# Kernel tuning notes

Hardware: AMD Instinct MI355X
Metric: run time of the kernel (lower is better)

## Reference

```python
import jax, jax.numpy as jnp
import numpy as np

B, T, I, H, L, S = 128, 256, 256, 256, 4, 3


def _gru(x_t, w_i, b_i, b_h):
    # torch.nn.GRUCell called WITHOUT hx in the source => hidden state is 0,
    # so Whh @ 0 vanishes and only the b_hh bias contributes to the gates.
    gi = x_t @ w_i.T + b_i                      # [B, 3H]
    hh = b_h.shape[0] // 3
    i_r, i_z, i_n = gi[:, :hh], gi[:, hh:2 * hh], gi[:, 2 * hh:]
    h_r, h_z, h_n = b_h[:hh], b_h[hh:2 * hh], b_h[2 * hh:]
    r = jax.nn.sigmoid(i_r + h_r)
    z = jax.nn.sigmoid(i_z + h_z)
    n = jnp.tanh(i_n + r * h_n)
    return (1.0 - z) * n                        # + z * 0


def setup_inputs() -> dict:
    key = jax.random.key(0)
    ks = jax.random.split(key, 12)
    s = 1.0 / np.sqrt(H)
    u = lambda k, shape: jax.random.uniform(k, shape, jnp.float32, -s, s)
    return {
        "x": jax.random.normal(ks[0], (B, T, I), jnp.float32),
        "hidden": jax.random.normal(ks[1], (B, L, L), jnp.float32),
        "w_ih0": u(ks[2], (S, 3 * H, I)),      # layer-0 input weights, per split
        "b_ih0": u(ks[3], (S, 3 * H)),
        "b_hh0": u(ks[4], (S, 3 * H)),
        "w_ih": u(ks[5], (S, L - 1, 3 * H, H)),  # layers 1..L-1
        "b_ih": u(ks[6], (S, L - 1, 3 * H)),
        "b_hh": u(ks[7], (S, L - 1, 3 * H)),
        "w_lw": u(ks[8], (L, H)),              # layer_weights: Linear(H -> L)
        "b_lw": u(ks[9], (L,)),
        "w_sel": u(ks[10], (S, H + I)),        # selective_layer: Linear(H+I -> S)
        "b_sel": u(ks[11], (S,)),
    }


def reference(x, hidden, w_ih0, b_ih0, b_hh0, w_ih, b_ih, b_hh, w_lw, b_lw, w_sel, b_sel):
    Lm1 = w_ih.shape[1]

    def run_stack(x_t, cur):
        # cur is a (possibly traced) int index selecting one of S GRU stacks
        hs = [_gru(x_t, w_ih0[cur], b_ih0[cur], b_hh0[cur])]
        for l in range(Lm1):
            hs.append(_gru(hs[-1], w_ih[cur, l], b_ih[cur, l], b_hh[cur, l]))
        return jnp.stack(hs, axis=1)            # [B, L, H]

    h0 = run_stack(x[:, 0, :], 0)               # first step always uses stack 0

    def step(h, x_t):
        energy = h @ w_lw.T + b_lw              # [B, L, L]
        attn = jnp.sum(hidden * energy, axis=2) # [B, L]
        a = jax.nn.softmax(attn, axis=1)
        ctx = jnp.einsum('bl,blh->bh', a, h)    # [B, H]
        scores = jnp.concatenate([ctx, x_t], axis=1) @ w_sel.T + b_sel  # [B, S]
        cur = jnp.argmax(jnp.sum(scores, axis=0))  # batch-summed routing
        h_new = run_stack(x_t, cur)
        return h_new, h_new[:, -1, :]

    h_final, ys = jax.lax.scan(step, h0, jnp.swapaxes(x[:, 1:, :], 0, 1))
    outputs = jnp.concatenate([h0[:, -1:, :], jnp.swapaxes(ys, 0, 1)], axis=1)  # [B, T, H]
    return outputs, h_final[:, -1, :]
```

## Files before the change

### kernel.cpp

```cpp
#include <hip/hip_runtime.h>
#include <math.h>

#define Bsz 128
#define Tsz 256
#define Isz 256
#define Hsz 256
#define Lsz 4
#define Ssz 3
#define Mrows (Bsz*Tsz)

using f16x8 = __attribute__((ext_vector_type(8))) _Float16;
using f32x4 = __attribute__((ext_vector_type(4))) float;

#define LOG2E 1.44269504f

__global__ __launch_bounds__(256) void f32_to_f16_3(
    const float* __restrict__ s0, _Float16* __restrict__ d0, int n0,
    const float* __restrict__ s1, _Float16* __restrict__ d1, int n1,
    const float* __restrict__ s2, _Float16* __restrict__ d2, int n2)
{
  int idx = blockIdx.x * 256 + threadIdx.x;
  const float* s; _Float16* d;
  if (idx < n0)           { s = s0; d = d0; }
  else if (idx < n0 + n1) { idx -= n0; s = s1; d = d1; }
  else                    { idx -= n0 + n1; if (idx >= n2) return; s = s2; d = d2; }
  const float4 v0 = *(const float4*)(s + (size_t)idx * 8);
  const float4 v1 = *(const float4*)(s + (size_t)idx * 8 + 4);
  _Float16 h[8];
  h[0] = (_Float16)v0.x; h[1] = (_Float16)v0.y;
  h[2] = (_Float16)v0.z; h[3] = (_Float16)v0.w;
  h[4] = (_Float16)v1.x; h[5] = (_Float16)v1.y;
  h[6] = (_Float16)v1.z; h[7] = (_Float16)v1.w;
  *(uint4*)(d + (size_t)idx * 8) = *(uint4*)h;
}

__global__ __launch_bounds__(256, 2) void gemm_gru_f16(
    const _Float16* __restrict__ Abase, size_t a_cur_stride,
    const _Float16* __restrict__ Wbase, size_t w_cur_stride,
    const float* __restrict__ bi_g, size_t bi_stride,
    const float* __restrict__ bh_g, size_t bh_stride,
    _Float16* __restrict__ Hout)
{
  __shared__ _Float16 AhS[3][8192];

  const int tid  = threadIdx.x;
  const int cu   = blockIdx.z;
  const int n0   = blockIdx.y * 64;
  const int rmb  = blockIdx.x * 512;

  const _Float16* A = Abase + (size_t)cu * a_cur_stride;
  const _Float16* W = Wbase + (size_t)cu * w_cur_stride;
  const float* bi = bi_g + (size_t)cu * bi_stride;
  const float* bh = bh_g + (size_t)cu * bh_stride;

  const int lane = tid & 63;
  const int wv   = tid >> 6;
  const int q    = lane >> 4;
  const int c    = lane & 15;

  const int ncol = n0 + wv * 16 + c;
  f16x8 wf[3][8];
  #pragma unroll
  for (int s = 0; s < 3; s++)
    #pragma unroll
    for (int k0 = 0; k0 < 8; k0++)
      wf[s][k0] = *(const f16x8*)(W + (size_t)(s * 256 + ncol) * 256 + k0 * 32 + q * 8);
  #pragma unroll
  for (int s = 0; s < 3; s++)
    #pragma unroll
    for (int k0 = 0; k0 < 8; k0++)
      asm volatile("" : "+v"(wf[s][k0]));

  const float c0  = -LOG2E * (bi[ncol] + bh[ncol]);
  const float c1  =  LOG2E * (bi[256 + ncol] + bh[256 + ncol]);
  const float c3  = 2.f * LOG2E * bi[512 + ncol];
  const float bhn = bh[512 + ncol];

  f32x4 acc[3][2];

  auto stage = [&](int buf, int ch) {
    const int rm = rmb + ch * 32;
    #pragma unroll
    for (int i = 0; i < 4; i++) {
      const int p0 = 8 * wv + 2 * i;
      const int pk = p0 + (lane >> 5);
      const _Float16* src = A + (size_t)(rm + (lane & 31)) * 256 + pk * 8;
      __builtin_amdgcn_global_load_lds(
          (const __attribute__((address_space(1))) void*)src,
          (__attribute__((address_space(3))) void*)&AhS[buf][p0 * 256],
          16, 0, 0);
    }
  };

  auto compute_chunk = [&](int buf, int ch) {
    const int rm = rmb + ch * 32;
    #pragma unroll
    for (int s = 0; s < 3; s++)
      #pragma unroll
      for (int mi = 0; mi < 2; mi++)
        acc[s][mi] = (f32x4)0.f;
    #pragma unroll
    for (int k0 = 0; k0 < 8; k0++) {
      const f16x8 a0 = *(const f16x8*)&AhS[buf][(k0 * 4 + q) * 256 + c * 8];
      const f16x8 a1 = *(const f16x8*)&AhS[buf][(k0 * 4 + q) * 256 + 128 + c * 8];
      #pragma unroll
      for (int s = 0; s < 3; s++) {
        acc[s][0] = __builtin_amdgcn_mfma_f32_16x16x32_f16(a0, wf[s][k0], acc[s][0], 0, 0, 0);
        acc[s][1] = __builtin_amdgcn_mfma_f32_16x16x32_f16(a1, wf[s][k0], acc[s][1], 0, 0, 0);
      }
    }
    #pragma unroll
    for (int mi = 0; mi < 2; mi++) {
      #pragma unroll
      for (int reg = 0; reg < 4; reg++) {
        const float ar = acc[0][mi][reg];
        const float az = acc[1][mi][reg];
        const float an = acc[2][mi][reg];
        const float e0 = __builtin_amdgcn_exp2f(fmaf(-LOG2E, ar, c0));
        const float r  = __builtin_amdgcn_rcpf(1.f + e0);
        const float e1 = __builtin_amdgcn_exp2f(fmaf(LOG2E, az, c1));
        const float tt = fmaf(r, bhn, an);
        const float a2 = fminf(fmaf(2.f * LOG2E, tt, c3), 120.f);
        const float e2 = __builtin_amdgcn_exp2f(a2);
        const float out = (e2 - 1.f) *
            __builtin_amdgcn_rcpf((1.f + e1) * (1.f + e2));
        const size_t row = (size_t)cu * Mrows + rm + mi * 16 + q * 4 + reg;
        Hout[row * 256 + ncol] = (_Float16)out;
      }
    }
  };

  stage(0, 0);
  stage(1, 1);
  asm volatile("s_waitcnt vmcnt(4)" ::: "memory");
  __builtin_amdgcn_s_barrier();

  int bc = 0;
  for (int t = 0; t < 14; ++t) {
    int bs = bc + 2; if (bs >= 3) bs -= 3;
    stage(bs, t + 2);
    compute_chunk(bc, t);
    asm volatile("s_waitcnt vmcnt(12)" ::: "memory");
    __builtin_amdgcn_s_barrier();
    bc = (bc + 1 == 3) ? 0 : bc + 1;
  }
  compute_chunk(bc, 14);
  asm volatile("s_waitcnt vmcnt(0)" ::: "memory");
  __builtin_amdgcn_s_barrier();
  bc = (bc + 1 == 3) ? 0 : bc + 1;
  compute_chunk(bc, 15);
}

__global__ __launch_bounds__(256) void ep_tile(
    const _Float16* __restrict__ Hh,
    const float* __restrict__ w_lw, const float* __restrict__ w_sel, int layer,
    float* __restrict__ e, float* __restrict__ p)
{
  __shared__ float wc[7][256];
  __shared__ float ps[4][64][8];
  const int tid = threadIdx.x;
  const size_t mg0 = (size_t)blockIdx.x * 64;

  #pragma unroll
  for (int j = 0; j < 7; j++)
    wc[j][tid] = (j < 4) ? w_lw[j * 256 + tid] : w_sel[(j - 4) * 512 + tid];
  __syncthreads();

  const int r = tid & 63, pp = tid >> 6;
  const _Float16* hrow = Hh + (mg0 + r) * 256 + pp * 64;
  float acc[7] = {0.f, 0.f, 0.f, 0.f, 0.f, 0.f, 0.f};
  #pragma unroll
  for (int i = 0; i < 8; i++) {
    union { uint4 u; _Float16 h[8]; } hv;
    hv.u = *(const uint4*)(hrow + i * 8);
    float hf[8];
    #pragma unroll
    for (int k = 0; k < 8; k++) hf[k] = (float)hv.h[k];
    #pragma unroll
    for (int j = 0; j < 7; j++) {
      const float4 w0 = *(const float4*)&wc[j][pp * 64 + i * 8];
      const float4 w1 = *(const float4*)&wc[j][pp * 64 + i * 8 + 4];
      acc[j] += hf[0] * w0.x + hf[1] * w0.y + hf[2] * w0.z + hf[3] * w0.w
              + hf[4] * w1.x + hf[5] * w1.y + hf[6] * w1.z + hf[7] * w1.w;
    }
  }
  #pragma unroll
  for (int j = 0; j < 7; j++) ps[pp][r][j] = acc[j];
  __syncthreads();

  if (tid < 64) {
    float d[7];
    #pragma unroll
    for (int j = 0; j < 7; j++)
      d[j] = ps[0][tid][j] + ps[1][tid][j] + ps[2][tid][j] + ps[3][tid][j];
    const size_t mg = mg0 + tid;
    const int cc = (int)(mg >> 15);
    const int m  = (int)(mg & 32767);
    const int b = m >> 8, t = m & 255;
    const size_t base = ((size_t)cc * Tsz + t) * Bsz + b;
    #pragma unroll
    for (int j = 0; j < 4; j++) e[base * 16 + layer * 4 + j] = d[j];
    #pragma unroll
    for (int j = 0; j < 3; j++) p[base * 12 + layer * 3 + j] = d[4 + j];
  }
}

__global__ __launch_bounds__(128) void attn_xs(
    const float* __restrict__ e, const float* __restrict__ p,
    const float* __restrict__ hidden, const float* __restrict__ b_lw,
    const float* __restrict__ x, const float* __restrict__ w_sel,
    const float* __restrict__ b_sel,
    float* __restrict__ score_h, float* __restrict__ xs)
{
  __shared__ float red[2][3];
  const int t = blockIdx.x;
  const int wv = threadIdx.x >> 6, ln = threadIdx.x & 63;

  if (blockIdx.y < 3) {
    const int cc = blockIdx.y;
    const int b = threadIdx.x;
    const float* eb = e + ((size_t)(cc * Tsz + t) * Bsz + b) * 16;
    const float* pb = p + ((size_t)(cc * Tsz + t) * Bsz + b) * 12;
    const float* hb = hidden + b * 16;
    const float bl0 = b_lw[0], bl1 = b_lw[1], bl2 = b_lw[2], bl3 = b_lw[3];
    float attn[4];
    #pragma unroll
    for (int i = 0; i < 4; i++) {
      attn[i] = hb[i * 4 + 0] * (eb[i * 4 + 0] + bl0)
              + hb[i * 4 + 1] * (eb[i * 4 + 1] + bl1)
              + hb[i * 4 + 2] * (eb[i * 4 + 2] + bl2)
              + hb[i * 4 + 3] * (eb[i * 4 + 3] + bl3);
    }
    const float mx = fmaxf(fmaxf(attn[0], attn[1]), fmaxf(attn[2], attn[3]));
    float ex[4], sum = 0.f;
    #pragma unroll
    for (int i = 0; i < 4; i++) { ex[i] = expf(attn[i] - mx); sum += ex[i]; }
    const float inv = 1.f / sum;
    float sc[3];
    #pragma unroll
    for (int s = 0; s < 3; s++) {
      float v = 0.f;
      #pragma unroll
      for (int i = 0; i < 4; i++) v += ex[i] * pb[i * 3 + s];
      sc[s] = v * inv;
    }
    #pragma unroll
    for (int off = 32; off; off >>= 1)
      #pragma unroll
      for (int s = 0; s < 3; s++) sc[s] += __shfl_xor(sc[s], off);
    if (ln == 0) { red[wv][0] = sc[0]; red[wv][1] = sc[1]; red[wv][2] = sc[2]; }
    __syncthreads();
    if (threadIdx.x == 0) {
      #pragma unroll
      for (int s = 0; s < 3; s++)
        score_h[((size_t)cc * Tsz + t) * 3 + s] = red[0][s] + red[1][s];
    }
  } else {
    const int k = threadIdx.x;
    float s0 = 0.f, s1 = 0.f;
    for (int b = 0; b < Bsz; b++) {
      const float* xb = x + ((size_t)b * Tsz + t) * Isz;
      s0 += xb[k]; s1 += xb[k + 128];
    }
    float pr[3];
    #pragma unroll
    for (int qq = 0; qq < 3; qq++)
      pr[qq] = s0 * w_sel[qq * (Hsz + Isz) + Hsz + k]
             + s1 * w_sel[qq * (Hsz + Isz) + Hsz + k + 128];
    #pragma unroll
    for (int off = 32; off; off >>= 1)
      #pragma unroll
      for (int qq = 0; qq < 3; qq++) pr[qq] += __shfl_xor(pr[qq], off);
    if (ln == 0) { red[wv][0] = pr[0]; red[wv][1] = pr[1]; red[wv][2] = pr[2]; }
    __syncthreads();
    if (threadIdx.x == 0) {
      #pragma unroll
      for (int qq = 0; qq < 3; qq++)
        xs[t * 3 + qq] = red[0][qq] + red[1][qq] + (float)Bsz * b_sel[qq];
    }
  }
}

__global__ __launch_bounds__(256) void select_kernel(
    const float* __restrict__ score_h, const float* __restrict__ xs,
    int* __restrict__ cur)
{
  __shared__ unsigned S[Tsz];
  const int t = threadIdx.x;

  unsigned m = 0x24;
  if (t >= 1) {
    m = 0;
    const float* xr = xs + t * 3;
    #pragma unroll
    for (int cc = 0; cc < 3; cc++) {
      const float* sh = score_h + ((size_t)cc * Tsz + (t - 1)) * 3;
      const float v0 = sh[0] + xr[0];
      const float v1 = sh[1] + xr[1];
      const float v2 = sh[2] + xr[2];
      unsigned best = 0; float bv = v0;
      if (v1 > bv) { bv = v1; best = 1; }
      if (v2 > bv) { bv = v2; best = 2; }
      m |= best << (2 * cc);
    }
  }
  S[t] = m;
  __syncthreads();

  #pragma unroll
  for (int d = 1; d < Tsz; d <<= 1) {
    const unsigned prev = (t >= d) ? S[t - d] : 0x24u;
    const unsigned self = S[t];
    __syncthreads();
    unsigned comp = 0;
    #pragma unroll
    for (int xx = 0; xx < 3; xx++) {
      const unsigned y = (prev >> (2 * xx)) & 3u;
      const unsigned z = (self >> (2 * y)) & 3u;
      comp |= z << (2 * xx);
    }
    S[t] = comp;
    __syncthreads();
  }
  cur[t] = (int)(S[t] & 3u);
}

__global__ __launch_bounds__(256) void gather_out(
    const _Float16* __restrict__ Hh, const int* __restrict__ cur,
    float* __restrict__ out)
{
  const size_t idx = ((size_t)blockIdx.x * 256 + threadIdx.x) * 4;
  const size_t BTH = (size_t)Bsz * Tsz * Hsz;
  int b, t, h;
  if (idx < BTH) {
    b = (int)(idx >> 16);
    const int rem = (int)(idx & 65535);
    t = rem >> 8; h = rem & 255;
  } else {
    const size_t r2 = idx - BTH;
    b = (int)(r2 >> 8); h = (int)(r2 & 255); t = Tsz - 1;
  }
  const int cc = cur[t];
  const size_t g = (((size_t)cc * Mrows + (size_t)b * Tsz + t) * Hsz + h);
  union { ushort4 u; _Float16 hv[4]; } cv;
  cv.u = *(const ushort4*)(Hh + g);
  float4 v;
  v.x = (float)cv.hv[0]; v.y = (float)cv.hv[1];
  v.z = (float)cv.hv[2]; v.w = (float)cv.hv[3];
  *(float4*)(out + idx) = v;
}

extern "C" void kernel_launch(void* const* d_in, const int* in_sizes, int n_in,
                              void* d_out, int out_size, void* d_ws, size_t ws_size,
                              hipStream_t stream) {
  const float* x      = (const float*)d_in[0];
  const float* hidden = (const float*)d_in[1];
  const float* w_ih0  = (const float*)d_in[2];
  const float* b_ih0  = (const float*)d_in[3];
  const float* b_hh0  = (const float*)d_in[4];
  const float* w_ih   = (const float*)d_in[5];
  const float* b_ih   = (const float*)d_in[6];
  const float* b_hh   = (const float*)d_in[7];
  const float* w_lw   = (const float*)d_in[8];
  const float* b_lw   = (const float*)d_in[9];
  const float* w_sel  = (const float*)d_in[10];
  const float* b_sel  = (const float*)d_in[11];
  float* out = (float*)d_out;

  char* w = (char*)d_ws;
  const size_t HN = (size_t)3 * Mrows * 256;
  const size_t XN = (size_t)Bsz * Tsz * Isz;
  const size_t W0N = (size_t)3 * 768 * 256;
  const size_t WLN = (size_t)3 * 3 * 768 * 256;
  _Float16* HA  = (_Float16*)w; w += HN * 2;
  _Float16* HB  = (_Float16*)w; w += HN * 2;
  _Float16* xh  = (_Float16*)w; w += XN * 2;
  _Float16* Wh0 = (_Float16*)w; w += W0N * 2;
  _Float16* WhL = (_Float16*)w; w += WLN * 2;
  float* e       = (float*)w; w += (size_t)3 * Tsz * Bsz * 16 * 4;
  float* p       = (float*)w; w += (size_t)3 * Tsz * Bsz * 12 * 4;
  float* score_h = (float*)w; w += (size_t)3 * Tsz * 3 * 4;
  float* xsb     = (float*)w; w += (size_t)Tsz * 3 * 4;
  int*   curb    = (int*)w;   w += (size_t)Tsz * 4;

  f32_to_f16_3<<<5248, 256, 0, stream>>>(
      x, xh, (int)(XN / 8),
      w_ih0, Wh0, (int)(W0N / 8),
      w_ih, WhL, (int)(WLN / 8));

  dim3 ggrid(64, 4, 3);

  gemm_gru_f16<<<ggrid, 256, 0, stream>>>(
      xh, (size_t)0, Wh0, (size_t)768 * 256,
      b_ih0, (size_t)768, b_hh0, (size_t)768, HA);
  ep_tile<<<(3 * Mrows) / 64, 256, 0, stream>>>(HA, w_lw, w_sel, 0, e, p);

  const size_t wcur = (size_t)3 * 768 * 256;
  const size_t bst  = (size_t)3 * 768;
  _Float16* ping = HA; _Float16* pong = HB;
  for (int l = 1; l < 4; l++) {
    gemm_gru_f16<<<ggrid, 256, 0, stream>>>(
        ping, (size_t)Mrows * 256,
        WhL + (size_t)(l - 1) * 768 * 256, wcur,
        b_ih + (size_t)(l - 1) * 768, bst,
        b_hh + (size_t)(l - 1) * 768, bst, pong);
    ep_tile<<<(3 * Mrows) / 64, 256, 0, stream>>>(pong, w_lw, w_sel, l, e, p);
    _Float16* t1 = ping; ping = pong; pong = t1;
  }

  attn_xs<<<dim3(Tsz, 4), 128, 0, stream>>>(
      e, p, hidden, b_lw, x, w_sel, b_sel, score_h, xsb);
  select_kernel<<<1, 256, 0, stream>>>(score_h, xsb, curb);
  gather_out<<<8224, 256, 0, stream>>>(ping, curb, out);
}
```

Measured before the change: 402.8 us.

## Fuse per-layer epilogue projection into next layer's GEMM launch as extra blocks

The GEMM kernel now uses a flat 1D grid. Blocks past the GEMM range compute the previous layer's energy and selection projections, which the separate ep_tile launch used to do. Each layer's projection therefore runs in the same launch as the next layer's GEMM, reading the same input activations. This removes three kernel launches and lets the small projection work overlap with the GEMM. The trade-off is a larger shared-memory declaration (48KB) for every block, which may reduce GEMM occupancy, and the final layer still needs a separate ep_tile.

New measurement: 365.5 us. -9.3%, faster.

```diff
diff --git a/kernel.cpp b/kernel.cpp
--- a/kernel.cpp
+++ b/kernel.cpp
@@ -13,6 +13,7 @@
 using f32x4 = __attribute__((ext_vector_type(4))) float;
 
 #define LOG2E 1.44269504f
+#define GEMM_BLOCKS 768
 
 __global__ __launch_bounds__(256) void f32_to_f16_3(
     const float* __restrict__ s0, _Float16* __restrict__ d0, int n0,
@@ -39,14 +40,69 @@
     const _Float16* __restrict__ Wbase, size_t w_cur_stride,
     const float* __restrict__ bi_g, size_t bi_stride,
     const float* __restrict__ bh_g, size_t bh_stride,
-    _Float16* __restrict__ Hout)
-{
-  __shared__ _Float16 AhS[3][8192];
-
-  const int tid  = threadIdx.x;
-  const int cu   = blockIdx.z;
-  const int n0   = blockIdx.y * 64;
-  const int rmb  = blockIdx.x * 512;
+    _Float16* __restrict__ Hout,
+    const float* __restrict__ w_lw, const float* __restrict__ w_sel,
+    float* __restrict__ e_out, float* __restrict__ p_out, int layer_ep)
+{
+  __shared__ __align__(16) char smem[49152];
+  const int tid = threadIdx.x;
+  const int bid = blockIdx.x;
+
+  if (bid >= GEMM_BLOCKS) {
+    float (*wc)[256]   = (float(*)[256])smem;
+    float (*ps)[64][8] = (float(*)[64][8])(smem + 7 * 256 * 4);
+    const size_t mg0 = (size_t)(bid - GEMM_BLOCKS) * 64;
+
+    #pragma unroll
+    for (int j = 0; j < 7; j++)
+      wc[j][tid] = (j < 4) ? w_lw[j * 256 + tid] : w_sel[(j - 4) * 512 + tid];
+    __syncthreads();
+
+    const int r = tid & 63, pp = tid >> 6;
+    const _Float16* hrow = Abase + (mg0 + r) * 256 + pp * 64;
+    float acc[7] = {0.f, 0.f, 0.f, 0.f, 0.f, 0.f, 0.f};
+    #pragma unroll
+    for (int i = 0; i < 8; i++) {
+      union { uint4 u; _Float16 h[8]; } hv;
+      hv.u = *(const uint4*)(hrow + i * 8);
+      float hf[8];
+      #pragma unroll
+      for (int k = 0; k < 8; k++) hf[k] = (float)hv.h[k];
+      #pragma unroll
+      for (int j = 0; j < 7; j++) {
+        const float4 w0 = *(const float4*)&wc[j][pp * 64 + i * 8];
+        const float4 w1 = *(const float4*)&wc[j][pp * 64 + i * 8 + 4];
+        acc[j] += hf[0] * w0.x + hf[1] * w0.y + hf[2] * w0.z + hf[3] * w0.w
+                + hf[4] * w1.x + hf[5] * w1.y + hf[6] * w1.z + hf[7] * w1.w;
+      }
+    }
+    #pragma unroll
+    for (int j = 0; j < 7; j++) ps[pp][r][j] = acc[j];
+    __syncthreads();
+
+    if (tid < 64) {
+      float d[7];
+      #pragma unroll
+      for (int j = 0; j < 7; j++)
+        d[j] = ps[0][tid][j] + ps[1][tid][j] + ps[2][tid][j] + ps[3][tid][j];
+      const size_t mg = mg0 + tid;
+      const int cc = (int)(mg >> 15);
+      const int m  = (int)(mg & 32767);
+      const int b = m >> 8, t = m & 255;
+      const size_t base = ((size_t)cc * Tsz + t) * Bsz + b;
+      #pragma unroll
+      for (int j = 0; j < 4; j++) e_out[base * 16 + layer_ep * 4 + j] = d[j];
+      #pragma unroll
+      for (int j = 0; j < 3; j++) p_out[base * 12 + layer_ep * 3 + j] = d[4 + j];
+    }
+    return;
+  }
+
+  const int cu   = bid >> 8;
+  const int n0   = ((bid >> 6) & 3) * 64;
+  const int rmb  = (bid & 63) * 512;
+
+  _Float16 (*AhS)[8192] = (_Float16(*)[8192])smem;
 
   const _Float16* A = Abase + (size_t)cu * a_cur_stride;
   const _Float16* W = Wbase + (size_t)cu * w_cur_stride;
@@ -388,25 +444,24 @@
       w_ih0, Wh0, (int)(W0N / 8),
       w_ih, WhL, (int)(WLN / 8));
 
-  dim3 ggrid(64, 4, 3);
-
-  gemm_gru_f16<<<ggrid, 256, 0, stream>>>(
+  gemm_gru_f16<<<GEMM_BLOCKS, 256, 0, stream>>>(
       xh, (size_t)0, Wh0, (size_t)768 * 256,
-      b_ih0, (size_t)768, b_hh0, (size_t)768, HA);
-  ep_tile<<<(3 * Mrows) / 64, 256, 0, stream>>>(HA, w_lw, w_sel, 0, e, p);
+      b_ih0, (size_t)768, b_hh0, (size_t)768, HA,
+      nullptr, nullptr, nullptr, nullptr, -1);
 
   const size_t wcur = (size_t)3 * 768 * 256;
   const size_t bst  = (size_t)3 * 768;
   _Float16* ping = HA; _Float16* pong = HB;
   for (int l = 1; l < 4; l++) {
-    gemm_gru_f16<<<ggrid, 256, 0, stream>>>(
+    gemm_gru_f16<<<GEMM_BLOCKS + 1536, 256, 0, stream>>>(
         ping, (size_t)Mrows * 256,
         WhL + (size_t)(l - 1) * 768 * 256, wcur,
         b_ih + (size_t)(l - 1) * 768, bst,
-        b_hh + (size_t)(l - 1) * 768, bst, pong);
-    ep_tile<<<(3 * Mrows) / 64, 256, 0, stream>>>(pong, w_lw, w_sel, l, e, p);
+        b_hh + (size_t)(l - 1) * 768, bst, pong,
+        w_lw, w_sel, e, p, l - 1);
     _Float16* t1 = ping; ping = pong; pong = t1;
   }
+  ep_tile<<<(3 * Mrows) / 64, 256, 0, stream>>>(ping, w_lw, w_sel, 3, e, p);
 
   attn_xs<<<dim3(Tsz, 4), 128, 0, stream>>>(
       e, p, hidden, b_lw, x, w_sel, b_sel, score_h, xsb);
```
